# Kernel tuning notes

Measured on AMD Instinct MI355X. Metric: run time of the kernel, lower is better.

Reference implementation:

```python
import jax, jax.numpy as jnp
import numpy as np

D_MODEL = 1024
N_HEADS = 16
D_HEAD = 64
INIT_RANGE = 0.02
IGNORE = -100000.0


def setup_inputs() -> dict:
    key = jax.random.key(0)
    ks = jax.random.split(key, 5)
    x = jax.random.normal(ks[0], (2, 2048, D_MODEL), dtype=jnp.float32)
    W_Q = jax.random.normal(ks[1], (N_HEADS, D_MODEL, D_HEAD), dtype=jnp.float32) * INIT_RANGE
    W_K = jax.random.normal(ks[2], (N_HEADS, D_MODEL, D_HEAD), dtype=jnp.float32) * INIT_RANGE
    W_V = jax.random.normal(ks[3], (N_HEADS, D_MODEL, D_HEAD), dtype=jnp.float32) * INIT_RANGE
    W_O = jax.random.normal(ks[4], (N_HEADS, D_HEAD, D_MODEL), dtype=jnp.float32) * INIT_RANGE
    b_Q = jnp.zeros((N_HEADS, D_HEAD), dtype=jnp.float32)
    b_K = jnp.zeros((N_HEADS, D_HEAD), dtype=jnp.float32)
    b_V = jnp.zeros((N_HEADS, D_HEAD), dtype=jnp.float32)
    b_O = jnp.zeros((D_MODEL,), dtype=jnp.float32)
    return {"normalized_resid_pre": x, "W_Q": W_Q, "W_K": W_K, "W_V": W_V,
            "W_O": W_O, "b_Q": b_Q, "b_K": b_K, "b_V": b_V, "b_O": b_O}


def reference(normalized_resid_pre, W_Q, W_K, W_V, W_O, b_Q, b_K, b_V, b_O):
    x = normalized_resid_pre  # [b, s, d_model]
    q = jnp.einsum('bsd,hde->bshe', x, W_Q) + b_Q  # [b, s, h, d_head]
    k = jnp.einsum('bsd,hde->bshe', x, W_K) + b_K
    v = jnp.einsum('bsd,hde->bshe', x, W_V) + b_V
    scores = jnp.einsum('bqhe,bkhe->bhqk', q, k) / jnp.sqrt(jnp.float32(D_HEAD))
    s = x.shape[1]
    causal = jnp.arange(s)[:, None] >= jnp.arange(s)[None, :]  # [q, k]
    scores = jnp.where(causal, scores, jnp.float32(IGNORE))
    pattern = jax.nn.softmax(scores, axis=-1)  # [b, h, q, k]
    z = jnp.einsum('bkhe,bhqk->bqhe', v, pattern)
    out = jnp.einsum('bqhe,hed->bqd', z, W_O) + b_O
    return out
```

## Files before the change

### kernel.cpp

```cpp
#include <hip/hip_runtime.h>

#define SEQ 2048
#define BATCH 2
#define DM 1024
#define NH 16
#define DH 64

typedef __bf16 bf16;
typedef __bf16 bf16x8 __attribute__((ext_vector_type(8)));
typedef __bf16 bf16x4 __attribute__((ext_vector_type(4)));
typedef float f32x4 __attribute__((ext_vector_type(4)));

#define MFMA16(a, b, c) __builtin_amdgcn_mfma_f32_16x16x32_bf16((a), (b), (c), 0, 0, 0)

#if __has_builtin(__builtin_amdgcn_exp2f)
#define EXP2(x) __builtin_amdgcn_exp2f(x)
#else
#define EXP2(x) exp2f(x)
#endif

#define QSCALE 0.18033688f

typedef __attribute__((address_space(3))) void lds_void;
typedef __attribute__((address_space(1))) void glb_void;
__device__ __forceinline__ void gld16(void* lds, const void* g) {
    __builtin_amdgcn_global_load_lds((const glb_void*)g, (lds_void*)lds, 16, 0, 0);
}

__global__ __launch_bounds__(256) void k_prep(const float* __restrict__ x,
                                              const float* __restrict__ WQ,
                                              const float* __restrict__ WK,
                                              const float* __restrict__ WV,
                                              const float* __restrict__ WO,
                                              bf16* __restrict__ xb,
                                              bf16* __restrict__ wT,
                                              bf16* __restrict__ woT) {
    int bx = blockIdx.x;
    int t = threadIdx.x;
    if (bx < 2048) {
        int g = bx * 256 + t;
        const float4* x4 = (const float4*)x;
        float4 a = x4[2 * g];
        float4 b = x4[2 * g + 1];
        bf16x8 o;
        o[0] = (bf16)a.x; o[1] = (bf16)a.y; o[2] = (bf16)a.z; o[3] = (bf16)a.w;
        o[4] = (bf16)b.x; o[5] = (bf16)b.y; o[6] = (bf16)b.z; o[7] = (bf16)b.w;
        *(bf16x8*)(xb + 8 * g) = o;
        return;
    }
    __shared__ bf16 T[64 * 65];
    if (bx < 2816) {
        int id = bx - 2048;
        int kt = id & 15, ph = id >> 4;
        int p = ph >> 4, h = ph & 15;
        const float* Wp = (p == 0) ? WQ : (p == 1) ? WK : WV;
        const float* src = Wp + ((size_t)h * DM + (size_t)kt * 64) * DH;
        for (int i = 0; i < 4; i++) {
            int c = t + 256 * i;
            int r = c >> 4;
            int col = (c & 15) * 4;
            float4 v = *(const float4*)&src[r * 64 + col];
            T[(col + 0) * 65 + r] = (bf16)v.x;
            T[(col + 1) * 65 + r] = (bf16)v.y;
            T[(col + 2) * 65 + r] = (bf16)v.z;
            T[(col + 3) * 65 + r] = (bf16)v.w;
        }
        __syncthreads();
        bf16* dst = wT + (size_t)ph * 64 * DM + (size_t)kt * 64;
        for (int i = 0; i < 2; i++) {
            int c = t + 256 * i;
            int e = c >> 3;
            int k0 = (c & 7) * 8;
            bf16x8 o;
            for (int j = 0; j < 8; j++) o[j] = T[e * 65 + k0 + j];
            *(bf16x8*)&dst[(size_t)e * DM + k0] = o;
        }
    } else {
        int id = bx - 2816;
        int ht = id & 15, dt = id >> 4;
        for (int i = 0; i < 4; i++) {
            int c = t + 256 * i;
            int r = c >> 4;
            int col = (c & 15) * 4;
            float4 v = *(const float4*)&WO[((size_t)(ht * 64 + r)) * DM + dt * 64 + col];
            T[(col + 0) * 65 + r] = (bf16)v.x;
            T[(col + 1) * 65 + r] = (bf16)v.y;
            T[(col + 2) * 65 + r] = (bf16)v.z;
            T[(col + 3) * 65 + r] = (bf16)v.w;
        }
        __syncthreads();
        for (int i = 0; i < 2; i++) {
            int c = t + 256 * i;
            int d = c >> 3;
            int h0 = (c & 7) * 8;
            bf16x8 o;
            for (int j = 0; j < 8; j++) o[j] = T[d * 65 + h0 + j];
            *(bf16x8*)&woT[((size_t)(dt * 64 + d)) * DM + ht * 64 + h0] = o;
        }
    }
}

__global__ __launch_bounds__(512, 2) void k_qkv(const bf16* __restrict__ xb,
                                                const bf16* __restrict__ wT,
                                                const float* __restrict__ bQ,
                                                const float* __restrict__ bK,
                                                const float* __restrict__ bV,
                                                bf16* __restrict__ Qb,
                                                bf16* __restrict__ Kb,
                                                bf16* __restrict__ VTf) {
    int mt = blockIdx.x, nt = blockIdx.y, p = blockIdx.z;
    __shared__ __align__(16) char sm[131072];
    int t = threadIdx.x;
    int lane = t & 63, w = t >> 6;
    int l15 = lane & 15, quad = lane >> 4;
    int wr = w >> 2, wc = w & 3;
    int m0 = mt * 256, n0 = nt * 256;

    int P0 = t * 16;
    int L0 = P0 ^ (((P0 >> 7) & 3) << 4);
    int row0 = L0 >> 6, kc0 = (L0 >> 4) & 3;
    int P1 = 8192 + t * 16;
    int L1 = P1 ^ (((P1 >> 7) & 3) << 4);
    int row1 = L1 >> 6, kc1 = (L1 >> 4) & 3;
    const bf16* gA0 = xb + (size_t)(m0 + row0) * DM + kc0 * 8;
    const bf16* gA1 = xb + (size_t)(m0 + row1) * DM + kc1 * 8;
    const bf16* gB0 = wT + (size_t)(p * 1024 + n0 + row0) * DM + kc0 * 8;
    const bf16* gB1 = wT + (size_t)(p * 1024 + n0 + row1) * DM + kc1 * 8;

    auto stage = [&](int ts, bool bsel) {
        char* sb = sm + (ts & 3) * 32768;
        int ko = ts * 32;
        if (!bsel) {
            gld16(sb + w * 1024, gA0 + ko);
            gld16(sb + 8192 + w * 1024, gA1 + ko);
        } else {
            gld16(sb + 16384 + w * 1024, gB0 + ko);
            gld16(sb + 16384 + 8192 + w * 1024, gB1 + ko);
        }
    };

    int aoff[8], boff[4];
#pragma unroll
    for (int mi = 0; mi < 8; mi++) {
        int row = wr * 128 + mi * 16 + l15;
        aoff[mi] = row * 64 + ((quad ^ ((row >> 1) & 3)) << 4);
    }
#pragma unroll
    for (int ni = 0; ni < 4; ni++) {
        int row = wc * 64 + ni * 16 + l15;
        boff[ni] = 16384 + row * 64 + ((quad ^ ((row >> 1) & 3)) << 4);
    }

    const f32x4 z4 = {0.f, 0.f, 0.f, 0.f};
    f32x4 acc[8][4];
#pragma unroll
    for (int mi = 0; mi < 8; mi++)
#pragma unroll
        for (int ni = 0; ni < 4; ni++) acc[mi][ni] = z4;

    auto kstep = [&](int tt, bool st) {
        const char* sb = sm + (tt & 3) * 32768;
        bf16x8 bfr[4], afr[4];
#pragma unroll
        for (int ni = 0; ni < 4; ni++) bfr[ni] = *(const bf16x8*)(sb + boff[ni]);
#pragma unroll
        for (int mi = 0; mi < 4; mi++) afr[mi] = *(const bf16x8*)(sb + aoff[mi]);
        if (st) stage(tt + 3, false);
        __builtin_amdgcn_s_setprio(1);
#pragma unroll
        for (int mi = 0; mi < 4; mi++)
#pragma unroll
            for (int ni = 0; ni < 4; ni++)
                acc[mi][ni] = MFMA16(afr[mi], bfr[ni], acc[mi][ni]);
        __builtin_amdgcn_s_setprio(0);
        bf16x8 afr2[4];
#pragma unroll
        for (int mi = 0; mi < 4; mi++) afr2[mi] = *(const bf16x8*)(sb + aoff[4 + mi]);
        if (st) stage(tt + 3, true);
        __builtin_amdgcn_s_setprio(1);
#pragma unroll
        for (int mi = 0; mi < 4; mi++)
#pragma unroll
            for (int ni = 0; ni < 4; ni++)
                acc[4 + mi][ni] = MFMA16(afr2[mi], bfr[ni], acc[4 + mi][ni]);
        __builtin_amdgcn_s_setprio(0);
    };

    stage(0, false); stage(0, true);
    stage(1, false); stage(1, true);
    stage(2, false); stage(2, true);

#pragma unroll 1
    for (int tt = 0; tt < 29; tt++) {
        asm volatile("s_waitcnt vmcnt(8)\n\ts_barrier" ::: "memory");
        __builtin_amdgcn_sched_barrier(0);
        kstep(tt, true);
    }
    asm volatile("s_waitcnt vmcnt(8)\n\ts_barrier" ::: "memory");
    __builtin_amdgcn_sched_barrier(0);
    kstep(29, false);
    asm volatile("s_waitcnt vmcnt(4)\n\ts_barrier" ::: "memory");
    __builtin_amdgcn_sched_barrier(0);
    kstep(30, false);
    asm volatile("s_waitcnt vmcnt(0)\n\ts_barrier" ::: "memory");
    __builtin_amdgcn_sched_barrier(0);
    kstep(31, false);

    int b = m0 >> 11;
    if (p < 2) {
        const float* bias = (p == 0) ? bQ : bK;
        bf16* dst = (p == 0) ? Qb : Kb;
        float scale = (p == 0) ? QSCALE : 1.0f;
#pragma unroll
        for (int ni = 0; ni < 4; ni++) {
            int he = n0 + wc * 64 + ni * 16 + l15;
            int h = he >> 6, e = he & 63;
            float bia = bias[he];
            size_t rb = (size_t)(b * NH + h) * SEQ * DH + e;
#pragma unroll
            for (int mi = 0; mi < 8; mi++)
#pragma unroll
                for (int r = 0; r < 4; r++) {
                    int s = ((m0 + wr * 128 + mi * 16 + quad * 4 + r) & 2047);
                    dst[rb + (size_t)s * DH] = (bf16)((acc[mi][ni][r] + bia) * scale);
                }
        }
    } else {
#pragma unroll
        for (int ni = 0; ni < 4; ni++) {
            int he = n0 + wc * 64 + ni * 16 + l15;
            int h = he >> 6;
            float bia = bV[he];
#pragma unroll
            for (int mi = 0; mi < 8; mi++) {
                int kvl = (mt & 7) * 256 + wr * 128 + mi * 16;
                int kt = kvl >> 7;
                int f = (mi >> 1) * 4 + ni;
                size_t base = (((size_t)(b * NH + h) * 16 + kt) * 16 + f) * 512
                              + (size_t)((quad << 4) | l15) * 8 + (mi & 1) * 4;
                bf16x4 o;
#pragma unroll
                for (int r = 0; r < 4; r++) o[r] = (bf16)(acc[mi][ni][r] + bia);
                *(bf16x4*)&VTf[base] = o;
            }
        }
    }
}

__global__ __launch_bounds__(512, 4) void k_attn(const bf16* __restrict__ Qb,
                                                 const bf16* __restrict__ Kb,
                                                 const bf16* __restrict__ VTf,
                                                 bf16* __restrict__ Zb) {
    int bh = blockIdx.x;
    int y = blockIdx.y;
    int qt = (y < 8) ? y : 23 - y;
    int h = bh & 15, b = bh >> 4;
    __shared__ __align__(16) bf16 Ks[2][16 * 512];
    __shared__ __align__(16) bf16 Vs[16 * 512];
    int t = threadIdx.x;
    int lane = t & 63, w = t >> 6;
    int l15 = lane & 15, quad = lane >> 4;

    const bf16* qbase = Qb + (size_t)bh * SEQ * DH;
    const bf16* kbase = Kb + (size_t)bh * SEQ * DH;
    const bf16* vfrag = VTf + (size_t)bh * 16 * 8192;

    int qr0 = qt * 128 + w * 16;
    bf16x8 aq[2];
    for (int ks = 0; ks < 2; ks++)
        aq[ks] = *(const bf16x8*)&qbase[(size_t)(qr0 + l15) * DH + ks * 32 + quad * 8];

    auto stageK = [&](int buf, int kt) {
        for (int i = 0; i < 2; i++) {
            int f = w * 2 + i;
            int ks = f >> 3, ni = f & 7;
            gld16(&Ks[buf][f * 512],
                  kbase + (size_t)(kt * 128 + ni * 16 + l15) * DH + ks * 32 + quad * 8);
        }
    };
    auto stageV = [&](int kt) {
        const bf16* vt = vfrag + (size_t)kt * 8192;
        for (int i = 0; i < 2; i++) {
            int f = w * 2 + i;
            gld16(&Vs[f * 512], vt + f * 512 + lane * 8);
        }
    };

    const bf16 one = (bf16)1.0f;
    const bf16x8 ones = {one, one, one, one, one, one, one, one};
    const f32x4 z4 = {0.f, 0.f, 0.f, 0.f};
    f32x4 acco[4], accd;
    for (int no = 0; no < 4; no++) acco[no] = z4;
    accd = z4;

    stageK(0, 0);

    for (int kt = 0; kt <= qt; kt++) {
        int buf = kt & 1;
        asm volatile("s_waitcnt vmcnt(0)\n\ts_barrier" ::: "memory");
        __builtin_amdgcn_sched_barrier(0);
        stageV(kt);
        if (kt < qt) stageK(buf ^ 1, kt + 1);
        const bf16* Kbuf = Ks[buf];

        f32x4 accs[8];
        for (int ni = 0; ni < 8; ni++) accs[ni] = z4;
        __builtin_amdgcn_s_setprio(1);
        for (int ks = 0; ks < 2; ks++)
            for (int ni = 0; ni < 8; ni++) {
                bf16x8 ak = *(const bf16x8*)&Kbuf[(ks * 8 + ni) * 512 + lane * 8];
                accs[ni] = MFMA16(ak, aq[ks], accs[ni]);
            }
        __builtin_amdgcn_s_setprio(0);

        if (kt == qt) {
            int ql = w * 16 + l15;
            for (int ni = 0; ni < 8; ni++) {
                int kvl = ni * 16 + quad * 4;
                for (int r = 0; r < 4; r++)
                    if (kvl + r > ql) accs[ni][r] = -1e30f;
            }
        }

        bf16x4 pt[8];
        for (int ni = 0; ni < 8; ni++)
            for (int r = 0; r < 4; r++)
                pt[ni][r] = (bf16)EXP2(accs[ni][r]);

        if (kt < qt) {
            asm volatile("s_waitcnt vmcnt(2)\n\ts_barrier" ::: "memory");
        } else {
            asm volatile("s_waitcnt vmcnt(0)\n\ts_barrier" ::: "memory");
        }
        __builtin_amdgcn_sched_barrier(0);

        __builtin_amdgcn_s_setprio(1);
        for (int p4 = 0; p4 < 4; p4++) {
            bf16x8 ap;
            for (int j = 0; j < 4; j++) {
                ap[j] = pt[2 * p4][j];
                ap[4 + j] = pt[2 * p4 + 1][j];
            }
            accd = MFMA16(ap, ones, accd);
            for (int no = 0; no < 4; no++) {
                bf16x8 bv = *(const bf16x8*)&Vs[(p4 * 4 + no) * 512 + lane * 8];
                acco[no] = MFMA16(ap, bv, acco[no]);
            }
        }
        __builtin_amdgcn_s_setprio(0);
    }

    for (int r = 0; r < 4; r++) {
        float inv = 1.0f / accd[r];
        int q = qr0 + quad * 4 + r;
        size_t rowbase = ((size_t)b * SEQ + q) * DM + h * DH;
        for (int no = 0; no < 4; no++)
            Zb[rowbase + no * 16 + l15] = (bf16)(acco[no][r] * inv);
    }
}

__global__ __launch_bounds__(256, 2) void k_out(const bf16* __restrict__ Zb,
                                                const bf16* __restrict__ woT,
                                                const float* __restrict__ bO,
                                                float* __restrict__ out) {
    int mt = blockIdx.x, nt = blockIdx.y;
    __shared__ __align__(16) char sm[65536];
    int t = threadIdx.x;
    int lane = t & 63, w = t >> 6;
    int l15 = lane & 15, quad = lane >> 4;
    int wr = w >> 1, wc = w & 1;
    int m0 = mt * 128, n0 = nt * 128;

    int P0 = t * 16;
    int L0 = P0 ^ (((P0 >> 7) & 3) << 4);
    int row0 = L0 >> 6, kc0 = (L0 >> 4) & 3;
    int P1 = 4096 + t * 16;
    int L1 = P1 ^ (((P1 >> 7) & 3) << 4);
    int row1 = L1 >> 6, kc1 = (L1 >> 4) & 3;
    const bf16* gA0 = Zb + (size_t)(m0 + row0) * DM + kc0 * 8;
    const bf16* gA1 = Zb + (size_t)(m0 + row1) * DM + kc1 * 8;
    const bf16* gB0 = woT + (size_t)(n0 + row0) * DM + kc0 * 8;
    const bf16* gB1 = woT + (size_t)(n0 + row1) * DM + kc1 * 8;

    auto stage = [&](int ts) {
        char* sb = sm + (ts & 3) * 16384;
        int ko = ts * 32;
        gld16(sb + w * 1024, gA0 + ko);
        gld16(sb + 4096 + w * 1024, gA1 + ko);
        gld16(sb + 8192 + w * 1024, gB0 + ko);
        gld16(sb + 8192 + 4096 + w * 1024, gB1 + ko);
    };

    int aoff[4], boff[4];
#pragma unroll
    for (int mi = 0; mi < 4; mi++) {
        int row = wr * 64 + mi * 16 + l15;
        aoff[mi] = row * 64 + ((quad ^ ((row >> 1) & 3)) << 4);
    }
#pragma unroll
    for (int ni = 0; ni < 4; ni++) {
        int row = wc * 64 + ni * 16 + l15;
        boff[ni] = 8192 + row * 64 + ((quad ^ ((row >> 1) & 3)) << 4);
    }

    const f32x4 z4 = {0.f, 0.f, 0.f, 0.f};
    f32x4 acc[4][4];
#pragma unroll
    for (int mi = 0; mi < 4; mi++)
#pragma unroll
        for (int ni = 0; ni < 4; ni++) acc[mi][ni] = z4;

    auto kstep = [&](int tt, bool st) {
        const char* sb = sm + (tt & 3) * 16384;
        bf16x8 bfr[4], afr[4];
#pragma unroll
        for (int ni = 0; ni < 4; ni++) bfr[ni] = *(const bf16x8*)(sb + boff[ni]);
#pragma unroll
        for (int mi = 0; mi < 4; mi++) afr[mi] = *(const bf16x8*)(sb + aoff[mi]);
        if (st) stage(tt + 3);
        __builtin_amdgcn_s_setprio(1);
#pragma unroll
        for (int mi = 0; mi < 4; mi++)
#pragma unroll
            for (int ni = 0; ni < 4; ni++)
                acc[mi][ni] = MFMA16(afr[mi], bfr[ni], acc[mi][ni]);
        __builtin_amdgcn_s_setprio(0);
    };

    stage(0); stage(1); stage(2);

#pragma unroll 1
    for (int tt = 0; tt < 29; tt++) {
        asm volatile("s_waitcnt vmcnt(8)\n\ts_barrier" ::: "memory");
        __builtin_amdgcn_sched_barrier(0);
        kstep(tt, true);
    }
    asm volatile("s_waitcnt vmcnt(8)\n\ts_barrier" ::: "memory");
    __builtin_amdgcn_sched_barrier(0);
    kstep(29, false);
    asm volatile("s_waitcnt vmcnt(4)\n\ts_barrier" ::: "memory");
    __builtin_amdgcn_sched_barrier(0);
    kstep(30, false);
    asm volatile("s_waitcnt vmcnt(0)\n\ts_barrier" ::: "memory");
    __builtin_amdgcn_sched_barrier(0);
    kstep(31, false);

#pragma unroll
    for (int ni = 0; ni < 4; ni++) {
        int d = n0 + wc * 64 + ni * 16 + l15;
        float bia = bO[d];
#pragma unroll
        for (int mi = 0; mi < 4; mi++)
#pragma unroll
            for (int r = 0; r < 4; r++) {
                int s = m0 + wr * 64 + mi * 16 + quad * 4 + r;
                out[(size_t)s * DM + d] = acc[mi][ni][r] + bia;
            }
    }
}

extern "C" void kernel_launch(void* const* d_in, const int* in_sizes, int n_in,
                              void* d_out, int out_size, void* d_ws, size_t ws_size,
                              hipStream_t stream) {
    const float* x  = (const float*)d_in[0];
    const float* WQ = (const float*)d_in[1];
    const float* WK = (const float*)d_in[2];
    const float* WV = (const float*)d_in[3];
    const float* WO = (const float*)d_in[4];
    const float* bQ = (const float*)d_in[5];
    const float* bK = (const float*)d_in[6];
    const float* bV = (const float*)d_in[7];
    const float* bO = (const float*)d_in[8];
    float* out = (float*)d_out;

    char* w = (char*)d_ws;
    bf16* xb    = (bf16*)(w + 0);
    bf16* wqkvT = (bf16*)(w + (8u << 20));
    bf16* woT   = (bf16*)(w + (14u << 20));
    bf16* Qb    = (bf16*)(w + (16u << 20));
    bf16* Kb    = (bf16*)(w + (24u << 20));
    bf16* VTf   = (bf16*)(w + (32u << 20));
    bf16* Zb    = (bf16*)(w + (40u << 20));

    k_prep<<<3072, 256, 0, stream>>>(x, WQ, WK, WV, WO, xb, wqkvT, woT);
    k_qkv<<<dim3(16, 4, 3), 512, 0, stream>>>(xb, wqkvT, bQ, bK, bV, Qb, Kb, VTf);
    k_attn<<<dim3(32, 16), 512, 0, stream>>>(Qb, Kb, VTf, Zb);
    k_out<<<dim3(32, 8), 256, 0, stream>>>(Zb, woT, bO, out);
}
```

Measured before the change: 160.4 us.

## Fuse four kernels into one persistent megakernel with software grid barriers

Replaces the prep, QKV projection, attention and output projection launches with a single persistent kernel of 256 blocks that walks through the stages, separated by atomic-counter grid barriers. Attention work is re-mapped so each block handles a pair of query tiles (qt and 15-qt) to balance the causal load. The aim is to remove launch gaps and inter-kernel tails. In exchange, stages that ran with more blocks or higher occupancy now run with launch_bounds(512,1) and fixed block counts; the QKV stage uses only 192 of 256 blocks, and the barriers depend on all blocks being co-resident.

```diff
diff --git a/kernel.cpp b/kernel.cpp
--- a/kernel.cpp
+++ b/kernel.cpp
@@ -27,435 +27,435 @@
     __builtin_amdgcn_global_load_lds((const glb_void*)g, (lds_void*)lds, 16, 0, 0);
 }
 
-__global__ __launch_bounds__(256) void k_prep(const float* __restrict__ x,
-                                              const float* __restrict__ WQ,
-                                              const float* __restrict__ WK,
-                                              const float* __restrict__ WV,
-                                              const float* __restrict__ WO,
-                                              bf16* __restrict__ xb,
-                                              bf16* __restrict__ wT,
-                                              bf16* __restrict__ woT) {
-    int bx = blockIdx.x;
-    int t = threadIdx.x;
-    if (bx < 2048) {
-        int g = bx * 256 + t;
-        const float4* x4 = (const float4*)x;
-        float4 a = x4[2 * g];
-        float4 b = x4[2 * g + 1];
-        bf16x8 o;
-        o[0] = (bf16)a.x; o[1] = (bf16)a.y; o[2] = (bf16)a.z; o[3] = (bf16)a.w;
-        o[4] = (bf16)b.x; o[5] = (bf16)b.y; o[6] = (bf16)b.z; o[7] = (bf16)b.w;
-        *(bf16x8*)(xb + 8 * g) = o;
-        return;
+__device__ __forceinline__ void gridbar(int* cnt, int* gen, int nblk) {
+    asm volatile("s_waitcnt vmcnt(0) lgkmcnt(0)" ::: "memory");
+    __syncthreads();
+    if (threadIdx.x == 0) {
+        __threadfence();
+        int g = atomicAdd(gen, 0);
+        int old = atomicAdd(cnt, 1);
+        if (old == nblk - 1) {
+            atomicExch(cnt, 0);
+            __threadfence();
+            atomicAdd(gen, 1);
+        } else {
+            while (atomicAdd(gen, 0) == g) __builtin_amdgcn_s_sleep(2);
+        }
+        __threadfence();
     }
-    __shared__ bf16 T[64 * 65];
-    if (bx < 2816) {
-        int id = bx - 2048;
-        int kt = id & 15, ph = id >> 4;
-        int p = ph >> 4, h = ph & 15;
-        const float* Wp = (p == 0) ? WQ : (p == 1) ? WK : WV;
-        const float* src = Wp + ((size_t)h * DM + (size_t)kt * 64) * DH;
-        for (int i = 0; i < 4; i++) {
-            int c = t + 256 * i;
-            int r = c >> 4;
-            int col = (c & 15) * 4;
-            float4 v = *(const float4*)&src[r * 64 + col];
-            T[(col + 0) * 65 + r] = (bf16)v.x;
-            T[(col + 1) * 65 + r] = (bf16)v.y;
-            T[(col + 2) * 65 + r] = (bf16)v.z;
-            T[(col + 3) * 65 + r] = (bf16)v.w;
-        }
-        __syncthreads();
-        bf16* dst = wT + (size_t)ph * 64 * DM + (size_t)kt * 64;
-        for (int i = 0; i < 2; i++) {
-            int c = t + 256 * i;
-            int e = c >> 3;
-            int k0 = (c & 7) * 8;
-            bf16x8 o;
-            for (int j = 0; j < 8; j++) o[j] = T[e * 65 + k0 + j];
-            *(bf16x8*)&dst[(size_t)e * DM + k0] = o;
-        }
-    } else {
-        int id = bx - 2816;
-        int ht = id & 15, dt = id >> 4;
-        for (int i = 0; i < 4; i++) {
-            int c = t + 256 * i;
-            int r = c >> 4;
-            int col = (c & 15) * 4;
-            float4 v = *(const float4*)&WO[((size_t)(ht * 64 + r)) * DM + dt * 64 + col];
-            T[(col + 0) * 65 + r] = (bf16)v.x;
-            T[(col + 1) * 65 + r] = (bf16)v.y;
-            T[(col + 2) * 65 + r] = (bf16)v.z;
-            T[(col + 3) * 65 + r] = (bf16)v.w;
-        }
-        __syncthreads();
-        for (int i = 0; i < 2; i++) {
-            int c = t + 256 * i;
-            int d = c >> 3;
-            int h0 = (c & 7) * 8;
-            bf16x8 o;
-            for (int j = 0; j < 8; j++) o[j] = T[d * 65 + h0 + j];
-            *(bf16x8*)&woT[((size_t)(dt * 64 + d)) * DM + ht * 64 + h0] = o;
-        }
-    }
+    __syncthreads();
 }
 
-__global__ __launch_bounds__(512, 2) void k_qkv(const bf16* __restrict__ xb,
-                                                const bf16* __restrict__ wT,
-                                                const float* __restrict__ bQ,
-                                                const float* __restrict__ bK,
-                                                const float* __restrict__ bV,
-                                                bf16* __restrict__ Qb,
-                                                bf16* __restrict__ Kb,
-                                                bf16* __restrict__ VTf) {
-    int mt = blockIdx.x, nt = blockIdx.y, p = blockIdx.z;
+__global__ __launch_bounds__(512, 1) void k_mega(
+    const float* __restrict__ x,  const float* __restrict__ WQ,
+    const float* __restrict__ WK, const float* __restrict__ WV,
+    const float* __restrict__ WO, const float* __restrict__ bQ,
+    const float* __restrict__ bK, const float* __restrict__ bV,
+    const float* __restrict__ bO, float* __restrict__ out,
+    bf16* __restrict__ xb, bf16* __restrict__ wT, bf16* __restrict__ woT,
+    bf16* __restrict__ Qb, bf16* __restrict__ Kb, bf16* __restrict__ VTf,
+    bf16* __restrict__ Zb, int* __restrict__ bar)
+{
     __shared__ __align__(16) char sm[131072];
+    int* bcnt = bar;
+    int* bgen = bar + 1;
+    int bid = blockIdx.x;
     int t = threadIdx.x;
     int lane = t & 63, w = t >> 6;
     int l15 = lane & 15, quad = lane >> 4;
-    int wr = w >> 2, wc = w & 3;
-    int m0 = mt * 256, n0 = nt * 256;
-
-    int P0 = t * 16;
-    int L0 = P0 ^ (((P0 >> 7) & 3) << 4);
-    int row0 = L0 >> 6, kc0 = (L0 >> 4) & 3;
-    int P1 = 8192 + t * 16;
-    int L1 = P1 ^ (((P1 >> 7) & 3) << 4);
-    int row1 = L1 >> 6, kc1 = (L1 >> 4) & 3;
-    const bf16* gA0 = xb + (size_t)(m0 + row0) * DM + kc0 * 8;
-    const bf16* gA1 = xb + (size_t)(m0 + row1) * DM + kc1 * 8;
-    const bf16* gB0 = wT + (size_t)(p * 1024 + n0 + row0) * DM + kc0 * 8;
-    const bf16* gB1 = wT + (size_t)(p * 1024 + n0 + row1) * DM + kc1 * 8;
-
-    auto stage = [&](int ts, bool bsel) {
-        char* sb = sm + (ts & 3) * 32768;
-        int ko = ts * 32;
-        if (!bsel) {
+
+    {
+        const float4* x4 = (const float4*)x;
+        for (int i = 0; i < 4; i++) {
+            int g = bid * 2048 + i * 512 + t;
+            float4 a = x4[2 * g];
+            float4 b = x4[2 * g + 1];
+            bf16x8 o;
+            o[0] = (bf16)a.x; o[1] = (bf16)a.y; o[2] = (bf16)a.z; o[3] = (bf16)a.w;
+            o[4] = (bf16)b.x; o[5] = (bf16)b.y; o[6] = (bf16)b.z; o[7] = (bf16)b.w;
+            *(bf16x8*)(xb + 8 * g) = o;
+        }
+        bf16* T = (bf16*)sm;
+        for (int i = 0; i < 4; i++) {
+            int u = bid * 4 + i;
+            __syncthreads();
+            if (u < 768) {
+                int kt = u & 15, ph = u >> 4;
+                int p = ph >> 4, h = ph & 15;
+                const float* Wp = (p == 0) ? WQ : (p == 1) ? WK : WV;
+                const float* src = Wp + ((size_t)h * DM + (size_t)kt * 64) * DH;
+                for (int ii = 0; ii < 2; ii++) {
+                    int c = t + 512 * ii;
+                    int r = c >> 4;
+                    int col = (c & 15) * 4;
+                    float4 v = *(const float4*)&src[r * 64 + col];
+                    T[(col + 0) * 65 + r] = (bf16)v.x;
+                    T[(col + 1) * 65 + r] = (bf16)v.y;
+                    T[(col + 2) * 65 + r] = (bf16)v.z;
+                    T[(col + 3) * 65 + r] = (bf16)v.w;
+                }
+                __syncthreads();
+                bf16* dst = wT + (size_t)ph * 64 * DM + (size_t)kt * 64;
+                int e = t >> 3;
+                int k0 = (t & 7) * 8;
+                bf16x8 o;
+                for (int j = 0; j < 8; j++) o[j] = T[e * 65 + k0 + j];
+                *(bf16x8*)&dst[(size_t)e * DM + k0] = o;
+            } else {
+                int id2 = u - 768;
+                int ht = id2 & 15, dt = id2 >> 4;
+                for (int ii = 0; ii < 2; ii++) {
+                    int c = t + 512 * ii;
+                    int r = c >> 4;
+                    int col = (c & 15) * 4;
+                    float4 v = *(const float4*)&WO[((size_t)(ht * 64 + r)) * DM + dt * 64 + col];
+                    T[(col + 0) * 65 + r] = (bf16)v.x;
+                    T[(col + 1) * 65 + r] = (bf16)v.y;
+                    T[(col + 2) * 65 + r] = (bf16)v.z;
+                    T[(col + 3) * 65 + r] = (bf16)v.w;
+                }
+                __syncthreads();
+                int d = t >> 3;
+                int h0 = (t & 7) * 8;
+                bf16x8 o;
+                for (int j = 0; j < 8; j++) o[j] = T[d * 65 + h0 + j];
+                *(bf16x8*)&woT[((size_t)(dt * 64 + d)) * DM + ht * 64 + h0] = o;
+            }
+        }
+    }
+    gridbar(bcnt, bgen, 256);
+
+    if (bid < 192) {
+        int mt = bid & 15, nt = (bid >> 4) & 3, p = bid >> 6;
+        int wr = w >> 2, wc = w & 3;
+        int m0 = mt * 256, n0 = nt * 256;
+
+        int P0 = t * 16;
+        int L0 = P0 ^ (((P0 >> 7) & 3) << 4);
+        int row0 = L0 >> 6, kc0 = (L0 >> 4) & 3;
+        int P1 = 8192 + t * 16;
+        int L1 = P1 ^ (((P1 >> 7) & 3) << 4);
+        int row1 = L1 >> 6, kc1 = (L1 >> 4) & 3;
+        const bf16* gA0 = xb + (size_t)(m0 + row0) * DM + kc0 * 8;
+        const bf16* gA1 = xb + (size_t)(m0 + row1) * DM + kc1 * 8;
+        const bf16* gB0 = wT + (size_t)(p * 1024 + n0 + row0) * DM + kc0 * 8;
+        const bf16* gB1 = wT + (size_t)(p * 1024 + n0 + row1) * DM + kc1 * 8;
+
+        auto stage = [&](int ts, bool bsel) {
+            char* sb = sm + (ts & 3) * 32768;
+            int ko = ts * 32;
+            if (!bsel) {
+                gld16(sb + w * 1024, gA0 + ko);
+                gld16(sb + 8192 + w * 1024, gA1 + ko);
+            } else {
+                gld16(sb + 16384 + w * 1024, gB0 + ko);
+                gld16(sb + 16384 + 8192 + w * 1024, gB1 + ko);
+            }
+        };
+
+        int aoff[8], boff[4];
+#pragma unroll
+        for (int mi = 0; mi < 8; mi++) {
+            int row = wr * 128 + mi * 16 + l15;
+            aoff[mi] = row * 64 + ((quad ^ ((row >> 1) & 3)) << 4);
+        }
+#pragma unroll
+        for (int ni = 0; ni < 4; ni++) {
+            int row = wc * 64 + ni * 16 + l15;
+            boff[ni] = 16384 + row * 64 + ((quad ^ ((row >> 1) & 3)) << 4);
+        }
+
+        const f32x4 z4 = {0.f, 0.f, 0.f, 0.f};
+        f32x4 acc[8][4];
+#pragma unroll
+        for (int mi = 0; mi < 8; mi++)
+#pragma unroll
+            for (int ni = 0; ni < 4; ni++) acc[mi][ni] = z4;
+
+        auto kstep = [&](int tt, bool st) {
+            const char* sb = sm + (tt & 3) * 32768;
+            bf16x8 bfr[4], afr[4];
+#pragma unroll
+            for (int ni = 0; ni < 4; ni++) bfr[ni] = *(const bf16x8*)(sb + boff[ni]);
+#pragma unroll
+            for (int mi = 0; mi < 4; mi++) afr[mi] = *(const bf16x8*)(sb + aoff[mi]);
+            if (st) stage(tt + 3, false);
+            __builtin_amdgcn_s_setprio(1);
+#pragma unroll
+            for (int mi = 0; mi < 4; mi++)
+#pragma unroll
+                for (int ni = 0; ni < 4; ni++)
+                    acc[mi][ni] = MFMA16(afr[mi], bfr[ni], acc[mi][ni]);
+            __builtin_amdgcn_s_setprio(0);
+            bf16x8 afr2[4];
+#pragma unroll
+            for (int mi = 0; mi < 4; mi++) afr2[mi] = *(const bf16x8*)(sb + aoff[4 + mi]);
+            if (st) stage(tt + 3, true);
+            __builtin_amdgcn_s_setprio(1);
+#pragma unroll
+            for (int mi = 0; mi < 4; mi++)
+#pragma unroll
+                for (int ni = 0; ni < 4; ni++)
+                    acc[4 + mi][ni] = MFMA16(afr2[mi], bfr[ni], acc[4 + mi][ni]);
+            __builtin_amdgcn_s_setprio(0);
+        };
+
+        stage(0, false); stage(0, true);
+        stage(1, false); stage(1, true);
+        stage(2, false); stage(2, true);
+
+#pragma unroll 1
+        for (int tt = 0; tt < 29; tt++) {
+            asm volatile("s_waitcnt vmcnt(8)\n\ts_barrier" ::: "memory");
+            __builtin_amdgcn_sched_barrier(0);
+            kstep(tt, true);
+        }
+        asm volatile("s_waitcnt vmcnt(8)\n\ts_barrier" ::: "memory");
+        __builtin_amdgcn_sched_barrier(0);
+        kstep(29, false);
+        asm volatile("s_waitcnt vmcnt(4)\n\ts_barrier" ::: "memory");
+        __builtin_amdgcn_sched_barrier(0);
+        kstep(30, false);
+        asm volatile("s_waitcnt vmcnt(0)\n\ts_barrier" ::: "memory");
+        __builtin_amdgcn_sched_barrier(0);
+        kstep(31, false);
+
+        int b = m0 >> 11;
+        if (p < 2) {
+            const float* bias = (p == 0) ? bQ : bK;
+            bf16* dst = (p == 0) ? Qb : Kb;
+            float scale = (p == 0) ? QSCALE : 1.0f;
+#pragma unroll
+            for (int ni = 0; ni < 4; ni++) {
+                int he = n0 + wc * 64 + ni * 16 + l15;
+                int h = he >> 6, e = he & 63;
+                float bia = bias[he];
+                size_t rb = (size_t)(b * NH + h) * SEQ * DH + e;
+#pragma unroll
+                for (int mi = 0; mi < 8; mi++)
+#pragma unroll
+                    for (int r = 0; r < 4; r++) {
+                        int s = ((m0 + wr * 128 + mi * 16 + quad * 4 + r) & 2047);
+                        dst[rb + (size_t)s * DH] = (bf16)((acc[mi][ni][r] + bia) * scale);
+                    }
+            }
+        } else {
+#pragma unroll
+            for (int ni = 0; ni < 4; ni++) {
+                int he = n0 + wc * 64 + ni * 16 + l15;
+                int h = he >> 6;
+                float bia = bV[he];
+#pragma unroll
+                for (int mi = 0; mi < 8; mi++) {
+                    int kvl = (mt & 7) * 256 + wr * 128 + mi * 16;
+                    int kt = kvl >> 7;
+                    int f = (mi >> 1) * 4 + ni;
+                    size_t base = (((size_t)(b * NH + h) * 16 + kt) * 16 + f) * 512
+                                  + (size_t)((quad << 4) | l15) * 8 + (mi & 1) * 4;
+                    bf16x4 o;
+#pragma unroll
+                    for (int r = 0; r < 4; r++) o[r] = (bf16)(acc[mi][ni][r] + bia);
+                    *(bf16x4*)&VTf[base] = o;
+                }
+            }
+        }
+    }
+    gridbar(bcnt, bgen, 256);
+
+    {
+        bf16 (*Ks)[16 * 512] = (bf16 (*)[16 * 512])sm;
+        bf16* Vs = (bf16*)(sm + 32768);
+        int bh = bid >> 3;
+        int jj = bid & 7;
+        int h = bh & 15, b = bh >> 4;
+        const bf16* qbase = Qb + (size_t)bh * SEQ * DH;
+        const bf16* kbase = Kb + (size_t)bh * SEQ * DH;
+        const bf16* vfrag = VTf + (size_t)bh * 16 * 8192;
+
+        for (int pass = 0; pass < 2; pass++) {
+            int qt = (pass == 0) ? jj : 15 - jj;
+            __syncthreads();
+
+            int qr0 = qt * 128 + w * 16;
+            bf16x8 aq[2];
+            for (int ks = 0; ks < 2; ks++)
+                aq[ks] = *(const bf16x8*)&qbase[(size_t)(qr0 + l15) * DH + ks * 32 + quad * 8];
+
+            auto stageK = [&](int buf, int kt) {
+                for (int i = 0; i < 2; i++) {
+                    int f = w * 2 + i;
+                    int ks = f >> 3, ni = f & 7;
+                    gld16(&Ks[buf][f * 512],
+                          kbase + (size_t)(kt * 128 + ni * 16 + l15) * DH + ks * 32 + quad * 8);
+                }
+            };
+            auto stageV = [&](int kt) {
+                const bf16* vt = vfrag + (size_t)kt * 8192;
+                for (int i = 0; i < 2; i++) {
+                    int f = w * 2 + i;
+                    gld16(&Vs[f * 512], vt + f * 512 + lane * 8);
+                }
+            };
+
+            const bf16 one = (bf16)1.0f;
+            const bf16x8 ones = {one, one, one, one, one, one, one, one};
+            const f32x4 z4 = {0.f, 0.f, 0.f, 0.f};
+            f32x4 acco[4], accd;
+            for (int no = 0; no < 4; no++) acco[no] = z4;
+            accd = z4;
+
+            stageK(0, 0);
+
+            for (int kt = 0; kt <= qt; kt++) {
+                int buf = kt & 1;
+                asm volatile("s_waitcnt vmcnt(0)\n\ts_barrier" ::: "memory");
+                __builtin_amdgcn_sched_barrier(0);
+                stageV(kt);
+                if (kt < qt) stageK(buf ^ 1, kt + 1);
+                const bf16* Kbuf = Ks[buf];
+
+                f32x4 accs[8];
+                for (int ni = 0; ni < 8; ni++) accs[ni] = z4;
+                __builtin_amdgcn_s_setprio(1);
+                for (int ks = 0; ks < 2; ks++)
+                    for (int ni = 0; ni < 8; ni++) {
+                        bf16x8 ak = *(const bf16x8*)&Kbuf[(ks * 8 + ni) * 512 + lane * 8];
+                        accs[ni] = MFMA16(ak, aq[ks], accs[ni]);
+                    }
+                __builtin_amdgcn_s_setprio(0);
+
+                if (kt == qt) {
+                    int ql = w * 16 + l15;
+                    for (int ni = 0; ni < 8; ni++) {
+                        int kvl = ni * 16 + quad * 4;
+                        for (int r = 0; r < 4; r++)
+                            if (kvl + r > ql) accs[ni][r] = -1e30f;
+                    }
+                }
+
+                bf16x4 pt[8];
+                for (int ni = 0; ni < 8; ni++)
+                    for (int r = 0; r < 4; r++)
+                        pt[ni][r] = (bf16)EXP2(accs[ni][r]);
+
+                if (kt < qt) {
+                    asm volatile("s_waitcnt vmcnt(2)\n\ts_barrier" ::: "memory");
+                } else {
+                    asm volatile("s_waitcnt vmcnt(0)\n\ts_barrier" ::: "memory");
+                }
+                __builtin_amdgcn_sched_barrier(0);
+
+                __builtin_amdgcn_s_setprio(1);
+                for (int p4 = 0; p4 < 4; p4++) {
+                    bf16x8 ap;
+                    for (int j = 0; j < 4; j++) {
+                        ap[j] = pt[2 * p4][j];
+                        ap[4 + j] = pt[2 * p4 + 1][j];
+                    }
+                    accd = MFMA16(ap, ones, accd);
+                    for (int no = 0; no < 4; no++) {
+                        bf16x8 bv = *(const bf16x8*)&Vs[(p4 * 4 + no) * 512 + lane * 8];
+                        acco[no] = MFMA16(ap, bv, acco[no]);
+                    }
+                }
+                __builtin_amdgcn_s_setprio(0);
+            }
+
+            for (int r = 0; r < 4; r++) {
+                float inv = 1.0f / accd[r];
+                int q = qr0 + quad * 4 + r;
+                size_t rowbase = ((size_t)b * SEQ + q) * DM + h * DH;
+                for (int no = 0; no < 4; no++)
+                    Zb[rowbase + no * 16 + l15] = (bf16)(acco[no][r] * inv);
+            }
+        }
+    }
+    gridbar(bcnt, bgen, 256);
+
+    {
+        int mt = bid & 31, nt = bid >> 5;
+        int wr = w >> 2, wc = w & 3;
+        int m0 = mt * 128, n0 = nt * 128;
+
+        int P0 = t * 16;
+        int L0 = P0 ^ (((P0 >> 7) & 3) << 4);
+        int row0 = L0 >> 6, kc0 = (L0 >> 4) & 3;
+        const bf16* gA0 = Zb + (size_t)(m0 + row0) * DM + kc0 * 8;
+        const bf16* gB0 = woT + (size_t)(n0 + row0) * DM + kc0 * 8;
+
+        auto stage = [&](int ts) {
+            char* sb = sm + (ts & 3) * 16384;
+            int ko = ts * 32;
             gld16(sb + w * 1024, gA0 + ko);
-            gld16(sb + 8192 + w * 1024, gA1 + ko);
-        } else {
-            gld16(sb + 16384 + w * 1024, gB0 + ko);
-            gld16(sb + 16384 + 8192 + w * 1024, gB1 + ko);
-        }
-    };
-
-    int aoff[8], boff[4];
-#pragma unroll
-    for (int mi = 0; mi < 8; mi++) {
-        int row = wr * 128 + mi * 16 + l15;
-        aoff[mi] = row * 64 + ((quad ^ ((row >> 1) & 3)) << 4);
-    }
-#pragma unroll
-    for (int ni = 0; ni < 4; ni++) {
-        int row = wc * 64 + ni * 16 + l15;
-        boff[ni] = 16384 + row * 64 + ((quad ^ ((row >> 1) & 3)) << 4);
-    }
-
-    const f32x4 z4 = {0.f, 0.f, 0.f, 0.f};
-    f32x4 acc[8][4];
-#pragma unroll
-    for (int mi = 0; mi < 8; mi++)
-#pragma unroll
-        for (int ni = 0; ni < 4; ni++) acc[mi][ni] = z4;
-
-    auto kstep = [&](int tt, bool st) {
-        const char* sb = sm + (tt & 3) * 32768;
-        bf16x8 bfr[4], afr[4];
-#pragma unroll
-        for (int ni = 0; ni < 4; ni++) bfr[ni] = *(const bf16x8*)(sb + boff[ni]);
-#pragma unroll
-        for (int mi = 0; mi < 4; mi++) afr[mi] = *(const bf16x8*)(sb + aoff[mi]);
-        if (st) stage(tt + 3, false);
-        __builtin_amdgcn_s_setprio(1);
+            gld16(sb + 8192 + w * 1024, gB0 + ko);
+        };
+
+        int aoff[4], boff[2];
+#pragma unroll
+        for (int mi = 0; mi < 4; mi++) {
+            int row = wr * 64 + mi * 16 + l15;
+            aoff[mi] = row * 64 + ((quad ^ ((row >> 1) & 3)) << 4);
+        }
+#pragma unroll
+        for (int ni = 0; ni < 2; ni++) {
+            int row = wc * 32 + ni * 16 + l15;
+            boff[ni] = 8192 + row * 64 + ((quad ^ ((row >> 1) & 3)) << 4);
+        }
+
+        const f32x4 z4 = {0.f, 0.f, 0.f, 0.f};
+        f32x4 acc[4][2];
 #pragma unroll
         for (int mi = 0; mi < 4; mi++)
 #pragma unroll
-            for (int ni = 0; ni < 4; ni++)
-                acc[mi][ni] = MFMA16(afr[mi], bfr[ni], acc[mi][ni]);
-        __builtin_amdgcn_s_setprio(0);
-        bf16x8 afr2[4];
-#pragma unroll
-        for (int mi = 0; mi < 4; mi++) afr2[mi] = *(const bf16x8*)(sb + aoff[4 + mi]);
-        if (st) stage(tt + 3, true);
-        __builtin_amdgcn_s_setprio(1);
-#pragma unroll
-        for (int mi = 0; mi < 4; mi++)
-#pragma unroll
-            for (int ni = 0; ni < 4; ni++)
-                acc[4 + mi][ni] = MFMA16(afr2[mi], bfr[ni], acc[4 + mi][ni]);
-        __builtin_amdgcn_s_setprio(0);
-    };
-
-    stage(0, false); stage(0, true);
-    stage(1, false); stage(1, true);
-    stage(2, false); stage(2, true);
+            for (int ni = 0; ni < 2; ni++) acc[mi][ni] = z4;
+
+        auto kstep = [&](int tt, bool st) {
+            const char* sb = sm + (tt & 3) * 16384;
+            bf16x8 bfr[2], afr[4];
+#pragma unroll
+            for (int ni = 0; ni < 2; ni++) bfr[ni] = *(const bf16x8*)(sb + boff[ni]);
+#pragma unroll
+            for (int mi = 0; mi < 4; mi++) afr[mi] = *(const bf16x8*)(sb + aoff[mi]);
+            if (st) stage(tt + 3);
+            __builtin_amdgcn_s_setprio(1);
+#pragma unroll
+            for (int mi = 0; mi < 4; mi++)
+#pragma unroll
+                for (int ni = 0; ni < 2; ni++)
+                    acc[mi][ni] = MFMA16(afr[mi], bfr[ni], acc[mi][ni]);
+            __builtin_amdgcn_s_setprio(0);
+        };
+
+        stage(0); stage(1); stage(2);
 
 #pragma unroll 1
-    for (int tt = 0; tt < 29; tt++) {
-        asm volatile("s_waitcnt vmcnt(8)\n\ts_barrier" ::: "memory");
-        __builtin_amdgcn_sched_barrier(0);
-        kstep(tt, true);
-    }
-    asm volatile("s_waitcnt vmcnt(8)\n\ts_barrier" ::: "memory");
-    __builtin_amdgcn_sched_barrier(0);
-    kstep(29, false);
-    asm volatile("s_waitcnt vmcnt(4)\n\ts_barrier" ::: "memory");
-    __builtin_amdgcn_sched_barrier(0);
-    kstep(30, false);
-    asm volatile("s_waitcnt vmcnt(0)\n\ts_barrier" ::: "memory");
-    __builtin_amdgcn_sched_barrier(0);
-    kstep(31, false);
-
-    int b = m0 >> 11;
-    if (p < 2) {
-        const float* bias = (p == 0) ? bQ : bK;
-        bf16* dst = (p == 0) ? Qb : Kb;
-        float scale = (p == 0) ? QSCALE : 1.0f;
-#pragma unroll
-        for (int ni = 0; ni < 4; ni++) {
-            int he = n0 + wc * 64 + ni * 16 + l15;
-            int h = he >> 6, e = he & 63;
-            float bia = bias[he];
-            size_t rb = (size_t)(b * NH + h) * SEQ * DH + e;
-#pragma unroll
-            for (int mi = 0; mi < 8; mi++)
+        for (int tt = 0; tt < 29; tt++) {
+            asm volatile("s_waitcnt vmcnt(4)\n\ts_barrier" ::: "memory");
+            __builtin_amdgcn_sched_barrier(0);
+            kstep(tt, true);
+        }
+        asm volatile("s_waitcnt vmcnt(4)\n\ts_barrier" ::: "memory");
+        __builtin_amdgcn_sched_barrier(0);
+        kstep(29, false);
+        asm volatile("s_waitcnt vmcnt(2)\n\ts_barrier" ::: "memory");
+        __builtin_amdgcn_sched_barrier(0);
+        kstep(30, false);
+        asm volatile("s_waitcnt vmcnt(0)\n\ts_barrier" ::: "memory");
+        __builtin_amdgcn_sched_barrier(0);
+        kstep(31, false);
+
+#pragma unroll
+        for (int ni = 0; ni < 2; ni++) {
+            int d = n0 + wc * 32 + ni * 16 + l15;
+            float bia = bO[d];
+#pragma unroll
+            for (int mi = 0; mi < 4; mi++)
 #pragma unroll
                 for (int r = 0; r < 4; r++) {
-                    int s = ((m0 + wr * 128 + mi * 16 + quad * 4 + r) & 2047);
-                    dst[rb + (size_t)s * DH] = (bf16)((acc[mi][ni][r] + bia) * scale);
-                }
-        }
-    } else {
-#pragma unroll
-        for (int ni = 0; ni < 4; ni++) {
-            int he = n0 + wc * 64 + ni * 16 + l15;
-            int h = he >> 6;
-            float bia = bV[he];
-#pragma unroll
-            for (int mi = 0; mi < 8; mi++) {
-                int kvl = (mt & 7) * 256 + wr * 128 + mi * 16;
-                int kt = kvl >> 7;
-                int f = (mi >> 1) * 4 + ni;
-                size_t base = (((size_t)(b * NH + h) * 16 + kt) * 16 + f) * 512
-                              + (size_t)((quad << 4) | l15) * 8 + (mi & 1) * 4;
-                bf16x4 o;
-#pragma unroll
-                for (int r = 0; r < 4; r++) o[r] = (bf16)(acc[mi][ni][r] + bia);
-                *(bf16x4*)&VTf[base] = o;
-            }
-        }
-    }
-}
-
-__global__ __launch_bounds__(512, 4) void k_attn(const bf16* __restrict__ Qb,
-                                                 const bf16* __restrict__ Kb,
-                                                 const bf16* __restrict__ VTf,
-                                                 bf16* __restrict__ Zb) {
-    int bh = blockIdx.x;
-    int y = blockIdx.y;
-    int qt = (y < 8) ? y : 23 - y;
-    int h = bh & 15, b = bh >> 4;
-    __shared__ __align__(16) bf16 Ks[2][16 * 512];
-    __shared__ __align__(16) bf16 Vs[16 * 512];
-    int t = threadIdx.x;
-    int lane = t & 63, w = t >> 6;
-    int l15 = lane & 15, quad = lane >> 4;
-
-    const bf16* qbase = Qb + (size_t)bh * SEQ * DH;
-    const bf16* kbase = Kb + (size_t)bh * SEQ * DH;
-    const bf16* vfrag = VTf + (size_t)bh * 16 * 8192;
-
-    int qr0 = qt * 128 + w * 16;
-    bf16x8 aq[2];
-    for (int ks = 0; ks < 2; ks++)
-        aq[ks] = *(const bf16x8*)&qbase[(size_t)(qr0 + l15) * DH + ks * 32 + quad * 8];
-
-    auto stageK = [&](int buf, int kt) {
-        for (int i = 0; i < 2; i++) {
-            int f = w * 2 + i;
-            int ks = f >> 3, ni = f & 7;
-            gld16(&Ks[buf][f * 512],
-                  kbase + (size_t)(kt * 128 + ni * 16 + l15) * DH + ks * 32 + quad * 8);
-        }
-    };
-    auto stageV = [&](int kt) {
-        const bf16* vt = vfrag + (size_t)kt * 8192;
-        for (int i = 0; i < 2; i++) {
-            int f = w * 2 + i;
-            gld16(&Vs[f * 512], vt + f * 512 + lane * 8);
-        }
-    };
-
-    const bf16 one = (bf16)1.0f;
-    const bf16x8 ones = {one, one, one, one, one, one, one, one};
-    const f32x4 z4 = {0.f, 0.f, 0.f, 0.f};
-    f32x4 acco[4], accd;
-    for (int no = 0; no < 4; no++) acco[no] = z4;
-    accd = z4;
-
-    stageK(0, 0);
-
-    for (int kt = 0; kt <= qt; kt++) {
-        int buf = kt & 1;
-        asm volatile("s_waitcnt vmcnt(0)\n\ts_barrier" ::: "memory");
-        __builtin_amdgcn_sched_barrier(0);
-        stageV(kt);
-        if (kt < qt) stageK(buf ^ 1, kt + 1);
-        const bf16* Kbuf = Ks[buf];
-
-        f32x4 accs[8];
-        for (int ni = 0; ni < 8; ni++) accs[ni] = z4;
-        __builtin_amdgcn_s_setprio(1);
-        for (int ks = 0; ks < 2; ks++)
-            for (int ni = 0; ni < 8; ni++) {
-                bf16x8 ak = *(const bf16x8*)&Kbuf[(ks * 8 + ni) * 512 + lane * 8];
-                accs[ni] = MFMA16(ak, aq[ks], accs[ni]);
-            }
-        __builtin_amdgcn_s_setprio(0);
-
-        if (kt == qt) {
-            int ql = w * 16 + l15;
-            for (int ni = 0; ni < 8; ni++) {
-                int kvl = ni * 16 + quad * 4;
-                for (int r = 0; r < 4; r++)
-                    if (kvl + r > ql) accs[ni][r] = -1e30f;
-            }
-        }
-
-        bf16x4 pt[8];
-        for (int ni = 0; ni < 8; ni++)
-            for (int r = 0; r < 4; r++)
-                pt[ni][r] = (bf16)EXP2(accs[ni][r]);
-
-        if (kt < qt) {
-            asm volatile("s_waitcnt vmcnt(2)\n\ts_barrier" ::: "memory");
-        } else {
-            asm volatile("s_waitcnt vmcnt(0)\n\ts_barrier" ::: "memory");
-        }
-        __builtin_amdgcn_sched_barrier(0);
-
-        __builtin_amdgcn_s_setprio(1);
-        for (int p4 = 0; p4 < 4; p4++) {
-            bf16x8 ap;
-            for (int j = 0; j < 4; j++) {
-                ap[j] = pt[2 * p4][j];
-                ap[4 + j] = pt[2 * p4 + 1][j];
-            }
-            accd = MFMA16(ap, ones, accd);
-            for (int no = 0; no < 4; no++) {
-                bf16x8 bv = *(const bf16x8*)&Vs[(p4 * 4 + no) * 512 + lane * 8];
-                acco[no] = MFMA16(ap, bv, acco[no]);
-            }
-        }
-        __builtin_amdgcn_s_setprio(0);
-    }
-
-    for (int r = 0; r < 4; r++) {
-        float inv = 1.0f / accd[r];
-        int q = qr0 + quad * 4 + r;
-        size_t rowbase = ((size_t)b * SEQ + q) * DM + h * DH;
-        for (int no = 0; no < 4; no++)
-            Zb[rowbase + no * 16 + l15] = (bf16)(acco[no][r] * inv);
-    }
-}
-
-__global__ __launch_bounds__(256, 2) void k_out(const bf16* __restrict__ Zb,
-                                                const bf16* __restrict__ woT,
-                                                const float* __restrict__ bO,
-                                                float* __restrict__ out) {
-    int mt = blockIdx.x, nt = blockIdx.y;
-    __shared__ __align__(16) char sm[65536];
-    int t = threadIdx.x;
-    int lane = t & 63, w = t >> 6;
-    int l15 = lane & 15, quad = lane >> 4;
-    int wr = w >> 1, wc = w & 1;
-    int m0 = mt * 128, n0 = nt * 128;
-
-    int P0 = t * 16;
-    int L0 = P0 ^ (((P0 >> 7) & 3) << 4);
-    int row0 = L0 >> 6, kc0 = (L0 >> 4) & 3;
-    int P1 = 4096 + t * 16;
-    int L1 = P1 ^ (((P1 >> 7) & 3) << 4);
-    int row1 = L1 >> 6, kc1 = (L1 >> 4) & 3;
-    const bf16* gA0 = Zb + (size_t)(m0 + row0) * DM + kc0 * 8;
-    const bf16* gA1 = Zb + (size_t)(m0 + row1) * DM + kc1 * 8;
-    const bf16* gB0 = woT + (size_t)(n0 + row0) * DM + kc0 * 8;
-    const bf16* gB1 = woT + (size_t)(n0 + row1) * DM + kc1 * 8;
-
-    auto stage = [&](int ts) {
-        char* sb = sm + (ts & 3) * 16384;
-        int ko = ts * 32;
-        gld16(sb + w * 1024, gA0 + ko);
-        gld16(sb + 4096 + w * 1024, gA1 + ko);
-        gld16(sb + 8192 + w * 1024, gB0 + ko);
-        gld16(sb + 8192 + 4096 + w * 1024, gB1 + ko);
-    };
-
-    int aoff[4], boff[4];
-#pragma unroll
-    for (int mi = 0; mi < 4; mi++) {
-        int row = wr * 64 + mi * 16 + l15;
-        aoff[mi] = row * 64 + ((quad ^ ((row >> 1) & 3)) << 4);
-    }
-#pragma unroll
-    for (int ni = 0; ni < 4; ni++) {
-        int row = wc * 64 + ni * 16 + l15;
-        boff[ni] = 8192 + row * 64 + ((quad ^ ((row >> 1) & 3)) << 4);
-    }
-
-    const f32x4 z4 = {0.f, 0.f, 0.f, 0.f};
-    f32x4 acc[4][4];
-#pragma unroll
-    for (int mi = 0; mi < 4; mi++)
-#pragma unroll
-        for (int ni = 0; ni < 4; ni++) acc[mi][ni] = z4;
-
-    auto kstep = [&](int tt, bool st) {
-        const char* sb = sm + (tt & 3) * 16384;
-        bf16x8 bfr[4], afr[4];
-#pragma unroll
-        for (int ni = 0; ni < 4; ni++) bfr[ni] = *(const bf16x8*)(sb + boff[ni]);
-#pragma unroll
-        for (int mi = 0; mi < 4; mi++) afr[mi] = *(const bf16x8*)(sb + aoff[mi]);
-        if (st) stage(tt + 3);
-        __builtin_amdgcn_s_setprio(1);
-#pragma unroll
-        for (int mi = 0; mi < 4; mi++)
-#pragma unroll
-            for (int ni = 0; ni < 4; ni++)
-                acc[mi][ni] = MFMA16(afr[mi], bfr[ni], acc[mi][ni]);
-        __builtin_amdgcn_s_setprio(0);
-    };
-
-    stage(0); stage(1); stage(2);
-
-#pragma unroll 1
-    for (int tt = 0; tt < 29; tt++) {
-        asm volatile("s_waitcnt vmcnt(8)\n\ts_barrier" ::: "memory");
-        __builtin_amdgcn_sched_barrier(0);
-        kstep(tt, true);
-    }
-    asm volatile("s_waitcnt vmcnt(8)\n\ts_barrier" ::: "memory");
-    __builtin_amdgcn_sched_barrier(0);
-    kstep(29, false);
-    asm volatile("s_waitcnt vmcnt(4)\n\ts_barrier" ::: "memory");
-    __builtin_amdgcn_sched_barrier(0);
-    kstep(30, false);
-    asm volatile("s_waitcnt vmcnt(0)\n\ts_barrier" ::: "memory");
-    __builtin_amdgcn_sched_barrier(0);
-    kstep(31, false);
-
-#pragma unroll
-    for (int ni = 0; ni < 4; ni++) {
-        int d = n0 + wc * 64 + ni * 16 + l15;
-        float bia = bO[d];
-#pragma unroll
-        for (int mi = 0; mi < 4; mi++)
-#pragma unroll
-            for (int r = 0; r < 4; r++) {
-                int s = m0 + wr * 64 + mi * 16 + quad * 4 + r;
-                out[(size_t)s * DM + d] = acc[mi][ni][r] + bia;
-            }
+                    int s = m0 + wr * 64 + mi * 16 + quad * 4 + r;
+                    out[(size_t)s * DM + d] = acc[mi][ni][r] + bia;
+                }
+        }
     }
 }
 
@@ -481,9 +481,9 @@
     bf16* Kb    = (bf16*)(w + (24u << 20));
     bf16* VTf   = (bf16*)(w + (32u << 20));
     bf16* Zb    = (bf16*)(w + (40u << 20));
-
-    k_prep<<<3072, 256, 0, stream>>>(x, WQ, WK, WV, WO, xb, wqkvT, woT);
-    k_qkv<<<dim3(16, 4, 3), 512, 0, stream>>>(xb, wqkvT, bQ, bK, bV, Qb, Kb, VTf);
-    k_attn<<<dim3(32, 16), 512, 0, stream>>>(Qb, Kb, VTf, Zb);
-    k_out<<<dim3(32, 8), 256, 0, stream>>>(Zb, woT, bO, out);
+    int*  bar   = (int*)(w + (48u << 20));
+
+    hipMemsetAsync(bar, 0, 64, stream);
+    k_mega<<<256, 512, 0, stream>>>(x, WQ, WK, WV, WO, bQ, bK, bV, bO, out,
+                                    xb, wqkvT, woT, Qb, Kb, VTf, Zb, bar);
 }
```

New measurement: 243.6 us. +51.9%, slower.
